# Kernel optimization log

Measured on AMD Instinct MI355X. Metric: run time of the kernel, lower is better.

Reference implementation:

```python
import math
import jax
import jax.numpy as jnp
import numpy as np

B = 4
SEQ_LEN = 512
ENC_IN = 21
TIME_DIM = 4
D_MODEL = 256
N_HEADS = 8
HEAD_DIM = D_MODEL // N_HEADS  # 32
NUM_K = 4
PATCH_LEN = 16
STRIDE = 8
EFF_LEN = (SEQ_LEN - PATCH_LEN) // STRIDE + 1  # 63, pad_len == 0
D_FF = 1024
PRED_LEN = 96
N_NEW = 2
N_ENC = 2
EPS = 1e-5


def setup_inputs() -> dict:
    key = jax.random.key(0)
    ks = iter(jax.random.split(key, 100))
    def nrm(shape, s=1.0):
        return jax.random.normal(next(ks), shape, jnp.float32) * s
    H, Dh, T, K = N_HEADS, HEAD_DIM, TIME_DIM, NUM_K
    inp = {}
    inp['x_enc'] = nrm((B, SEQ_LEN, ENC_IN))
    inp['x_mark_enc'] = jax.random.uniform(next(ks), (B, SEQ_LEN, TIME_DIM), jnp.float32)
    inp['x_dec'] = nrm((B, 144, ENC_IN))
    inp['x_mark_dec'] = jax.random.uniform(next(ks), (B, 144, TIME_DIM), jnp.float32)
    # DataEmbedding2: token conv (circular, k=3, no bias); positional enc is computed analytically
    inp['tok_W'] = nrm((D_MODEL, ENC_IN, 3), 0.05)
    # PatchEmbedding conv
    inp['patch_W'] = nrm((D_MODEL, D_MODEL, PATCH_LEN), 0.02)
    inp['patch_b'] = jnp.zeros((D_MODEL,), jnp.float32)
    # TimeKernelAttentionA layers (stacked on leading axis)
    inp['nl_WQ'] = nrm((N_NEW, D_MODEL, D_MODEL), 0.05)
    inp['nl_WK'] = nrm((N_NEW, D_MODEL, D_MODEL), 0.05)
    inp['nl_WV'] = nrm((N_NEW, D_MODEL, D_MODEL), 0.05)
    inp['nl_WO'] = nrm((N_NEW, D_MODEL, D_MODEL), 0.05)
    inp['nl_bO'] = jnp.zeros((N_NEW, D_MODEL), jnp.float32)
    inp['nl_mu_abs'] = nrm((N_NEW, H, Dh, T, K))
    inp['nl_sigma_abs'] = jnp.abs(nrm((N_NEW, H, Dh, T, K))) + 0.5
    inp['nl_w_abs'] = nrm((N_NEW, H, Dh, T, K), 0.1)
    inp['nl_mu_rel'] = nrm((N_NEW, H, Dh, T, K))
    inp['nl_sigma_rel'] = jnp.abs(nrm((N_NEW, H, Dh, T, K))) + 0.5
    inp['nl_w_rel'] = nrm((N_NEW, H, Dh, T, K), 0.1)
    inp['nl_alpha'] = jnp.ones((N_NEW, H), jnp.float32)
    inp['nl_beta'] = jnp.ones((N_NEW, H), jnp.float32)
    inp['nl_gamma'] = jnp.zeros((N_NEW, H), jnp.float32)
    # DataEmbedding_inverted: Linear(EFF_LEN -> d_model)
    inp['inv_W'] = nrm((D_MODEL, EFF_LEN), 0.05)
    inp['inv_b'] = jnp.zeros((D_MODEL,), jnp.float32)
    # Encoder layers (stacked)
    inp['el_Wq'] = nrm((N_ENC, D_MODEL, D_MODEL), 0.05)
    inp['el_bq'] = jnp.zeros((N_ENC, D_MODEL), jnp.float32)
    inp['el_Wk'] = nrm((N_ENC, D_MODEL, D_MODEL), 0.05)
    inp['el_bk'] = jnp.zeros((N_ENC, D_MODEL), jnp.float32)
    inp['el_Wv'] = nrm((N_ENC, D_MODEL, D_MODEL), 0.05)
    inp['el_bv'] = jnp.zeros((N_ENC, D_MODEL), jnp.float32)
    inp['el_Wo'] = nrm((N_ENC, D_MODEL, D_MODEL), 0.05)
    inp['el_bo'] = jnp.zeros((N_ENC, D_MODEL), jnp.float32)
    inp['el_W1'] = nrm((N_ENC, D_FF, D_MODEL), 0.05)
    inp['el_b1'] = jnp.zeros((N_ENC, D_FF), jnp.float32)
    inp['el_W2'] = nrm((N_ENC, D_MODEL, D_FF), 0.05)
    inp['el_b2'] = jnp.zeros((N_ENC, D_MODEL), jnp.float32)
    inp['el_n1_g'] = jnp.ones((N_ENC, D_MODEL), jnp.float32)
    inp['el_n1_b'] = jnp.zeros((N_ENC, D_MODEL), jnp.float32)
    inp['el_n2_g'] = jnp.ones((N_ENC, D_MODEL), jnp.float32)
    inp['el_n2_b'] = jnp.zeros((N_ENC, D_MODEL), jnp.float32)
    inp['norm_g'] = jnp.ones((D_MODEL,), jnp.float32)
    inp['norm_b'] = jnp.zeros((D_MODEL,), jnp.float32)
    inp['proj_W'] = nrm((PRED_LEN, D_MODEL), 0.05)
    inp['proj_b'] = jnp.zeros((PRED_LEN,), jnp.float32)
    return inp


def _conv1d(x, w, stride):
    # x: [B, Cin, L], w: [Cout, Cin, k]
    return jax.lax.conv_general_dilated(x, w, (stride,), 'VALID', dimension_numbers=('NCH', 'OIH', 'NCH'))


def _ln(x, g, b):
    m = x.mean(-1, keepdims=True)
    v = jnp.var(x, axis=-1, keepdims=True)
    return (x - m) / jnp.sqrt(v + EPS) * g + b


def _gauss(t, mu, sigma, w):
    # t: [B, N, T]; mu/sigma/w: [H, D, T, K] -> [B, H, D, N] (sum over T, K)
    diff = t[:, None, None, :, :, None] - mu[None, :, :, None, :, :]
    g = w[None, :, :, None, :, :] * jnp.exp(-(diff * diff) / (2.0 * sigma[None, :, :, None, :, :] ** 2))
    return g.sum((-1, -2))


def _tka(x, t, WQ, WK, WV, WO, bO, mu_a, sg_a, w_a, mu_r, sg_r, w_r, alpha, beta, gamma):
    Bn, L, _ = x.shape
    H, Dh = N_HEADS, HEAD_DIM
    q = (x @ WQ.T).reshape(Bn, L, H, Dh).transpose(0, 2, 1, 3)
    k = (x @ WK.T).reshape(Bn, L, H, Dh).transpose(0, 2, 1, 3)
    v = (x @ WV.T).reshape(Bn, L, H, Dh).transpose(0, 2, 1, 3)
    Xh = x.reshape(Bn, L, H, Dh).transpose(0, 2, 1, 3)
    Pij = jnp.einsum('bhid,bhjd->bhij', Xh, Xh)
    g_abs = _gauss(t, mu_a, sg_a, w_a)  # [B,H,D,L]
    t_rel = jnp.abs(t[:, :, None, :] - t[:, None, :, :]).reshape(Bn, L * L, TIME_DIM)
    g_rel = _gauss(t_rel, mu_r, sg_r, w_r).reshape(Bn, H, Dh, L, L).mean(2)  # [B,H,L,L]
    gi = g_abs.mean(2)  # [B,H,L]
    # NOTE: in the original, g_abs_j = g_abs_i.unsqueeze(-1).expand(...,L) (constant over j),
    # so (g_abs_i.unsqueeze(-1) + g_abs_j) == 2 * g_abs_i broadcast over j. We preserve that.
    a = alpha[None, :, None, None]
    b = beta[None, :, None, None]
    c = gamma[None, :, None, None]
    A = a * Pij * (2.0 * gi[..., None]) + b * Pij * g_rel + c
    scores = jnp.einsum('bhid,bhjd->bhij', q, k) / math.sqrt(Dh) * A
    attn = jax.nn.softmax(scores, axis=-1)
    out = jnp.einsum('bhij,bhjd->bhid', attn, v).transpose(0, 2, 1, 3).reshape(Bn, L, D_MODEL)
    return out @ WO.T + bO


def reference(x_enc, x_mark_enc, x_dec, x_mark_dec, tok_W, patch_W, patch_b, nl_WQ, nl_WK, nl_WV, nl_WO, nl_bO, nl_mu_abs, nl_sigma_abs, nl_w_abs, nl_mu_rel, nl_sigma_rel, nl_w_rel, nl_alpha, nl_beta, nl_gamma, inv_W, inv_b, el_Wq, el_bq, el_Wk, el_bk, el_Wv, el_bv, el_Wo, el_bo, el_W1, el_b1, el_W2, el_b2, el_n1_g, el_n1_b, el_n2_g, el_n2_b, norm_g, norm_b, proj_W, proj_b):
    # --- instance normalization (use_norm) ---
    means = x_enc.mean(1, keepdims=True)
    x = x_enc - means
    stdev = jnp.sqrt(jnp.var(x, axis=1, keepdims=True) + EPS)
    x = x / stdev
    # --- DataEmbedding2: TokenEmbedding (circular conv k=3) + sinusoidal PE, x_mark=None ---
    xc = x.transpose(0, 2, 1)  # [B, C, L]
    xp = jnp.concatenate([xc[:, :, -1:], xc, xc[:, :, :1]], axis=2)  # circular pad 1
    val = _conv1d(xp, tok_W, 1).transpose(0, 2, 1)  # [B, L, d]
    pos = jnp.arange(SEQ_LEN, dtype=jnp.float32)[:, None]
    div = jnp.exp(jnp.arange(0, D_MODEL, 2, dtype=jnp.float32) * (-math.log(10000.0) / D_MODEL))
    pe = jnp.zeros((SEQ_LEN, D_MODEL), jnp.float32)
    pe = pe.at[:, 0::2].set(jnp.sin(pos * div)).at[:, 1::2].set(jnp.cos(pos * div))
    enc = val + pe[None]
    # --- PatchEmbedding (pad_len == 0 for these dims) ---
    enc = _conv1d(enc.transpose(0, 2, 1), patch_W, STRIDE).transpose(0, 2, 1) + patch_b  # [B, 63, d]
    idx = jnp.arange(EFF_LEN)[:, None] * STRIDE + jnp.arange(PATCH_LEN)[None, :]
    t = x_mark_enc[:, idx, :].mean(2)  # [B, 63, T] (unfold + mean)
    # --- TimeKernelAttentionA stack ---
    for i in range(N_NEW):
        enc = _tka(enc, t, nl_WQ[i], nl_WK[i], nl_WV[i], nl_WO[i], nl_bO[i], nl_mu_abs[i], nl_sigma_abs[i], nl_w_abs[i], nl_mu_rel[i], nl_sigma_rel[i], nl_w_rel[i], nl_alpha[i], nl_beta[i], nl_gamma[i])
    # --- DataEmbedding_inverted ---
    xi = jnp.concatenate([enc.transpose(0, 2, 1), t.transpose(0, 2, 1)], axis=1)  # [B, d+T, 63]
    enc = xi @ inv_W.T + inv_b  # [B, d+T, d]
    # --- Encoder (FullAttention + FFN) ---
    Bn, Nt, _ = enc.shape
    for i in range(N_ENC):
        q = (enc @ el_Wq[i].T + el_bq[i]).reshape(Bn, Nt, N_HEADS, HEAD_DIM)
        k = (enc @ el_Wk[i].T + el_bk[i]).reshape(Bn, Nt, N_HEADS, HEAD_DIM)
        v = (enc @ el_Wv[i].T + el_bv[i]).reshape(Bn, Nt, N_HEADS, HEAD_DIM)
        sc = jnp.einsum('blhe,bshe->bhls', q, k) / math.sqrt(HEAD_DIM)
        attn = jax.nn.softmax(sc, axis=-1)
        o = jnp.einsum('bhls,bshd->blhd', attn, v).reshape(Bn, Nt, D_MODEL)
        o = o @ el_Wo[i].T + el_bo[i]
        xn = _ln(enc + o, el_n1_g[i], el_n1_b[i])
        y = jax.nn.gelu(xn @ el_W1[i].T + el_b1[i], approximate=False)
        y = y @ el_W2[i].T + el_b2[i]
        enc = _ln(xn + y, el_n2_g[i], el_n2_b[i])
    enc = _ln(enc, norm_g, norm_b)
    # --- projector + de-normalization ---
    dec = (enc @ proj_W.T + proj_b).transpose(0, 2, 1)[:, :, :ENC_IN]  # [B, pred_len, N]
    dec = dec * stdev[:, 0, :][:, None, :] + means[:, 0, :][:, None, :]
    return dec[:, -PRED_LEN:, :]
```

## Files before the change

kernel.cpp:

```cpp
#include <hip/hip_runtime.h>
#include <hip/hip_bf16.h>

#define NB 4
#define SEQ 512
#define CIN 21
#define TDIM 4
#define DM 256
#define NH 8
#define PLEN 16
#define PSTR 8
#define EL 63
#define DFF 1024
#define PRED 96
#define NT 260
#define EPSV 1e-5f

#define T_nlWQ 0
#define T_nlWK 131072
#define T_nlWV 262144
#define T_nlWO 393216
#define T_elWq 524288
#define T_elWk 655360
#define T_elWv 786432
#define T_elWo 917504
#define T_elW1 1048576
#define T_elW2 1572864
#define T_inv  2097152
#define T_proj 2113280
#define T_tok  2137856
#define T_pat  2153984

__device__ __forceinline__ float2 meanvar256(float v, float* sb) {
  __syncthreads();
  float s1 = v, s2 = v * v;
  #pragma unroll
  for (int off = 32; off > 0; off >>= 1) {
    s1 += __shfl_down(s1, off, 64);
    s2 += __shfl_down(s2, off, 64);
  }
  int wid = threadIdx.x >> 6, lane = threadIdx.x & 63;
  if (lane == 0) { sb[wid * 2] = s1; sb[wid * 2 + 1] = s2; }
  __syncthreads();
  float m = (sb[0] + sb[2] + sb[4] + sb[6]) * (1.0f / 256.0f);
  float q = (sb[1] + sb[3] + sb[5] + sb[7]) * (1.0f / 256.0f);
  return make_float2(m, q - m * m);
}

__device__ __forceinline__ void load16f(const float* p, float* o) {
  const float4* q = reinterpret_cast<const float4*>(p);
  float4 a = q[0], b = q[1], c = q[2], d = q[3];
  o[0]=a.x; o[1]=a.y; o[2]=a.z; o[3]=a.w;
  o[4]=b.x; o[5]=b.y; o[6]=b.z; o[7]=b.w;
  o[8]=c.x; o[9]=c.y; o[10]=c.z; o[11]=c.w;
  o[12]=d.x; o[13]=d.y; o[14]=d.z; o[15]=d.w;
}

__device__ __forceinline__ float dot32(const float4* a, const float4* b) {
  float s = 0.f;
  #pragma unroll
  for (int i = 0; i < 8; ++i) {
    float4 x = a[i], y = b[i];
    s += x.x*y.x + x.y*y.y + x.z*y.z + x.w*y.w;
  }
  return s;
}

__global__ void __launch_bounds__(256) k_prep(
    const float* __restrict__ nlWQ, const float* __restrict__ nlWK,
    const float* __restrict__ nlWV, const float* __restrict__ nlWO,
    const float* __restrict__ eWq, const float* __restrict__ eWk,
    const float* __restrict__ eWv, const float* __restrict__ eWo,
    const float* __restrict__ eW1, const float* __restrict__ eW2,
    const float* __restrict__ invW, const float* __restrict__ projW,
    const float* __restrict__ tokW, const float* __restrict__ patW,
    float* __restrict__ wt,
    const float* __restrict__ x, const float* __restrict__ xm,
    float* __restrict__ means, float* __restrict__ stdev,
    float* __restrict__ tout,
    const float* __restrict__ mu_r, const float* __restrict__ sg_r,
    const float* __restrict__ w_r,
    const float* __restrict__ mu_a, const float* __restrict__ sg_a,
    const float* __restrict__ w_a,
    float* __restrict__ grel, float* __restrict__ gib) {
  __shared__ float smem[32 * 33];
  int blk = blockIdx.x;
  int t = threadIdx.x;

  if (blk < 3128) {
    const float* src; float* dst; int R, C, tr, tc;
    if (blk < 1024) {
      int m = blk >> 6, tile = blk & 63;
      tr = tile >> 3; tc = tile & 7; R = 256; C = 256;
      int p = m >> 1, l = m & 1;
      const float* bases[8] = {nlWQ, nlWK, nlWV, nlWO, eWq, eWk, eWv, eWo};
      const int offs[8] = {T_nlWQ, T_nlWK, T_nlWV, T_nlWO, T_elWq, T_elWk, T_elWv, T_elWo};
      src = bases[p] + l * 65536;
      dst = wt + offs[p] + l * 65536;
    } else if (blk < 1536) {
      int q = blk - 1024; int l = q >> 8, s = q & 255;
      tr = s >> 3; tc = s & 7; R = 1024; C = 256;
      src = eW1 + l * 262144; dst = wt + T_elW1 + l * 262144;
    } else if (blk < 2048) {
      int q = blk - 1536; int l = q >> 8, s = q & 255;
      tr = s >> 5; tc = s & 31; R = 256; C = 1024;
      src = eW2 + l * 262144; dst = wt + T_elW2 + l * 262144;
    } else if (blk < 3072) {
      int q = blk - 2048; tr = q >> 7; tc = q & 127; R = 256; C = 4096;
      src = patW; dst = wt + T_pat;
    } else if (blk < 3088) {
      int q = blk - 3072; tr = q >> 1; tc = q & 1; R = 256; C = 63;
      src = invW; dst = wt + T_inv;
    } else if (blk < 3112) {
      int q = blk - 3088; tr = q >> 3; tc = q & 7; R = 96; C = 256;
      src = projW; dst = wt + T_proj;
    } else {
      int q = blk - 3112; tr = q >> 1; tc = q & 1; R = 256; C = 63;
      src = tokW; dst = wt + T_tok;
    }
    float (*ts)[33] = (float(*)[33])smem;
    int tx = t & 31, ty = t >> 5;
    #pragma unroll
    for (int i = 0; i < 4; ++i) {
      int r = tr * 32 + ty + i * 8, c = tc * 32 + tx;
      ts[ty + i * 8][tx] = (c < C) ? src[(size_t)r * C + c] : 0.f;
    }
    __syncthreads();
    #pragma unroll
    for (int i = 0; i < 4; ++i) {
      int c = tc * 32 + ty + i * 8, r = tr * 32 + tx;
      if (c < C) dst[(size_t)c * R + r] = ts[tx][ty + i * 8];
    }
  } else if (blk < 3216) {
    int sblk = blk - 3128;
    if (sblk < NB * CIN) {
      int b = sblk / CIN, c = sblk % CIN;
      const float* p = x + (size_t)b * SEQ * CIN + c;
      float v0 = p[t * CIN];
      float v1 = p[(t + 256) * CIN];
      float s1 = v0 + v1, s2 = v0 * v0 + v1 * v1;
      float* sb = smem;
      #pragma unroll
      for (int off = 32; off > 0; off >>= 1) {
        s1 += __shfl_down(s1, off, 64);
        s2 += __shfl_down(s2, off, 64);
      }
      int wid = t >> 6, lane = t & 63;
      if (lane == 0) { sb[wid * 2] = s1; sb[wid * 2 + 1] = s2; }
      __syncthreads();
      if (t == 0) {
        float a = sb[0] + sb[2] + sb[4] + sb[6];
        float q = sb[1] + sb[3] + sb[5] + sb[7];
        float m = a * (1.0f / 512.0f);
        float var = q * (1.0f / 512.0f) - m * m;
        means[sblk] = m;
        stdev[sblk] = sqrtf(var + EPSV);
      }
    } else {
      int idx = (sblk - NB * CIN) * 256 + t;
      if (idx >= NB * EL * TDIM) return;
      int b = idx / (EL * TDIM), r = idx % (EL * TDIM);
      int l = r >> 2, ti = r & 3;
      const float* p = xm + (size_t)b * SEQ * TDIM + (size_t)l * PSTR * TDIM + ti;
      float s = 0.f;
      #pragma unroll
      for (int k = 0; k < PLEN; ++k) s += p[k * TDIM];
      tout[idx] = s * (1.f / 16.f);
    }
  } else {
    int gblk = blk - 3216;
    int L = gblk / (NB * 252);
    int rem0 = gblk % (NB * 252);
    int b = rem0 / 252, chunk = rem0 % 252;
    int po = L * 4096;
    float* grelL = grel + (size_t)L * (NB * NH * EL * EL);
    float* gibL  = gib + (size_t)L * (NB * NH * EL);
    int h = t >> 5, dh = t & 31;
    float* s_t = smem;
    if (t < EL * TDIM) {
      int l = t >> 2, ti = t & 3;
      const float* p = xm + (size_t)b * SEQ * TDIM + (size_t)l * PSTR * TDIM + ti;
      float s = 0.f;
      #pragma unroll
      for (int k = 0; k < PLEN; ++k) s += p[k * TDIM];
      s_t[t] = s * (1.f / 16.f);
    }
    float pm[16], pc[16], pw[16];
    load16f(mu_r + po + (size_t)t * 16, pm);
    load16f(sg_r + po + (size_t)t * 16, pc);
    load16f(w_r  + po + (size_t)t * 16, pw);
    #pragma unroll
    for (int p = 0; p < 16; ++p) pc[p] = -0.5f / (pc[p] * pc[p]);
    __syncthreads();
    #pragma unroll 1
    for (int q = 0; q < 8; ++q) {
      int p = chunk * 8 + q;
      int i = (int)((127.0f - sqrtf(16129.0f - 8.0f * (float)p)) * 0.5f);
      while (i * (127 - i) / 2 > p) --i;
      while ((i + 1) * (126 - i) / 2 <= p) ++i;
      int j = i + (p - i * (127 - i) / 2);
      float dvv[4];
      dvv[0] = fabsf(s_t[i*4+0] - s_t[j*4+0]);
      dvv[1] = fabsf(s_t[i*4+1] - s_t[j*4+1]);
      dvv[2] = fabsf(s_t[i*4+2] - s_t[j*4+2]);
      dvv[3] = fabsf(s_t[i*4+3] - s_t[j*4+3]);
      float srel = 0.f;
      #pragma unroll
      for (int tt = 0; tt < 4; ++tt)
        #pragma unroll
        for (int k = 0; k < 4; ++k) {
          int pp = tt * 4 + k;
          float df = dvv[tt] - pm[pp];
          srel += pw[pp] * __expf(pc[pp] * df * df);
        }
      #pragma unroll
      for (int m = 1; m < 32; m <<= 1) srel += __shfl_xor(srel, m, 64);
      if (dh == 0) {
        float v = srel * (1.f / 32.f);
        grelL[(((size_t)b * NH + h) * EL + i) * EL + j] = v;
        grelL[(((size_t)b * NH + h) * EL + j) * EL + i] = v;
      }
    }
    if (chunk < EL) {
      load16f(mu_a + po + (size_t)t * 16, pm);
      load16f(sg_a + po + (size_t)t * 16, pc);
      load16f(w_a  + po + (size_t)t * 16, pw);
      #pragma unroll
      for (int p = 0; p < 16; ++p) pc[p] = -0.5f / (pc[p] * pc[p]);
      int i = chunk;
      float tiv[4] = {s_t[i*4+0], s_t[i*4+1], s_t[i*4+2], s_t[i*4+3]};
      float sabs = 0.f;
      #pragma unroll
      for (int tt = 0; tt < 4; ++tt)
        #pragma unroll
        for (int k = 0; k < 4; ++k) {
          int pp = tt * 4 + k;
          float df = tiv[tt] - pm[pp];
          sabs += pw[pp] * __expf(pc[pp] * df * df);
        }
      #pragma unroll
      for (int m = 1; m < 32; m <<= 1) sabs += __shfl_xor(sabs, m, 64);
      if (dh == 0) gibL[((size_t)b * NH + h) * EL + i] = sabs * (1.f / 32.f);
    }
  }
}

__global__ void __launch_bounds__(256) k_tokconv(
    const float* __restrict__ x, const float* __restrict__ tokWT,
    const float* __restrict__ means, const float* __restrict__ stdev,
    float* __restrict__ enc1) {
  int bi = blockIdx.x;
  int b = bi >> 6, sg = bi & 63;
  int s0 = sg * 8;
  __shared__ float sxr[10 * CIN];
  int t = threadIdx.x;
  if (t < 10 * CIN) {
    int li = t / CIN, c = t % CIN;
    int row = (s0 - 1 + li + SEQ) & 511;
    sxr[t] = (x[(size_t)b * SEQ * CIN + row * CIN + c] - means[b * CIN + c])
             / stdev[b * CIN + c];
  }
  __syncthreads();
  int d = t;
  float wreg[63];
  #pragma unroll
  for (int q = 0; q < 63; ++q) wreg[q] = tokWT[q * DM + d];
  int de = d & ~1;
  float dv = expf((float)de * (-9.210340371976184f / 256.0f));
  bool isodd = (d & 1);
  #pragma unroll 1
  for (int k = 0; k < 8; ++k) {
    float acc = 0.f;
    const float* sr = sxr + k * CIN;
    #pragma unroll
    for (int c = 0; c < CIN; ++c) {
      acc += sr[c]           * wreg[c * 3 + 0];
      acc += sr[CIN + c]     * wreg[c * 3 + 1];
      acc += sr[2 * CIN + c] * wreg[c * 3 + 2];
    }
    float ang = (float)(s0 + k) * dv;
    float pe = isodd ? cosf(ang) : sinf(ang);
    enc1[((size_t)b * SEQ + s0 + k) * DM + d] = acc + pe;
  }
}

__global__ void __launch_bounds__(256) k_patch_part(
    const float* __restrict__ enc1, const float* __restrict__ pWT,
    float* __restrict__ pbuf) {
  int bi = blockIdx.x;
  int pg = bi >> 3, kc = bi & 7;
  int p0 = pg * 6;
  __shared__ __align__(16) float sA[6 * 32 * 20];
  int t = threadIdx.x;
  for (int idx = t; idx < 6 * 32 * PLEN; idx += 256) {
    int pp = idx >> 9;
    int rem = idx & 511;
    int c = rem >> 4, k = rem & 15;
    int p = p0 + pp;
    int b = p / EL, l = p % EL;
    sA[pp * 640 + c * 20 + k] =
        enc1[((size_t)b * SEQ + l * PSTR + k) * DM + kc * 32 + c];
  }
  __syncthreads();
  int d = t;
  const float* wb = pWT + (size_t)(kc * 32 * PLEN) * DM + d;
  float acc[6] = {0.f, 0.f, 0.f, 0.f, 0.f, 0.f};
  #pragma unroll 1
  for (int kk0 = 0; kk0 < 512; kk0 += 8) {
    float w[8];
    #pragma unroll
    for (int q = 0; q < 8; ++q) w[q] = wb[(size_t)(kk0 + q) * DM];
    #pragma unroll
    for (int q = 0; q < 8; ++q) {
      int kk = kk0 + q;
      const float* sa = sA + (kk >> 4) * 20 + (kk & 15);
      acc[0] += sa[0 * 640] * w[q];
      acc[1] += sa[1 * 640] * w[q];
      acc[2] += sa[2 * 640] * w[q];
      acc[3] += sa[3 * 640] * w[q];
      acc[4] += sa[4 * 640] * w[q];
      acc[5] += sa[5 * 640] * w[q];
    }
  }
  const int S = NB * EL * DM;
  #pragma unroll
  for (int pp = 0; pp < 6; ++pp)
    pbuf[(size_t)kc * S + (size_t)(p0 + pp) * DM + d] = acc[pp];
}

__global__ void k_patch_red(const float* __restrict__ pbuf, const float* __restrict__ pb,
                            float* __restrict__ encP) {
  int p = blockIdx.x, t = threadIdx.x;
  const int S = NB * EL * DM;
  float v = 0.f;
  #pragma unroll
  for (int s = 0; s < 8; ++s) v += pbuf[(size_t)s * S + (size_t)p * DM + t];
  encP[(size_t)p * DM + t] = v + pb[t];
}

template<int R>
__global__ void __launch_bounds__(256) k_qkv2(
    const float* __restrict__ WqT, const float* __restrict__ WkT,
    const float* __restrict__ WvT,
    const float* __restrict__ bq, const float* __restrict__ bk,
    const float* __restrict__ bv,
    const float* __restrict__ xin,
    float* __restrict__ qo, float* __restrict__ ko, float* __restrict__ vo) {
  int bi = blockIdx.x;
  int rg = bi / 3, mat = bi % 3;
  int row0 = rg * R;
  __shared__ __align__(16) float sx[R * DM];
  __shared__ __align__(16) float sp[3 * R * DM];
  int t = threadIdx.x;
  int colg = t & 63, kq = t >> 6;
  #pragma unroll
  for (int i = 0; i < R / 4; ++i)
    reinterpret_cast<float4*>(sx)[t + i * 256] =
        reinterpret_cast<const float4*>(xin + (size_t)row0 * DM)[t + i * 256];
  __syncthreads();
  const float* WT = (mat == 0) ? WqT : (mat == 1) ? WkT : WvT;
  const float* bias = (mat == 0) ? bq : (mat == 1) ? bk : bv;
  float* out = (mat == 0) ? qo : (mat == 1) ? ko : vo;
  float acc[R][4];
  #pragma unroll
  for (int r = 0; r < R; ++r) { acc[r][0]=0.f; acc[r][1]=0.f; acc[r][2]=0.f; acc[r][3]=0.f; }
  const float* xb = sx + kq * 64;
  const float4* wp = reinterpret_cast<const float4*>(WT + (size_t)(kq * 64) * DM) + colg;
  #pragma unroll 1
  for (int k0 = 0; k0 < 64; k0 += 4) {
    float4 w[4];
    #pragma unroll
    for (int q = 0; q < 4; ++q) w[q] = wp[(size_t)(k0 + q) * 64];
    #pragma unroll
    for (int q = 0; q < 4; ++q)
      #pragma unroll
      for (int r = 0; r < R; ++r) {
        float xv = xb[r * DM + k0 + q];
        acc[r][0] += xv * w[q].x; acc[r][1] += xv * w[q].y;
        acc[r][2] += xv * w[q].z; acc[r][3] += xv * w[q].w;
      }
  }
  if (kq) {
    #pragma unroll
    for (int r = 0; r < R; ++r)
      reinterpret_cast<float4*>(sp)[((kq - 1) * R + r) * 64 + colg] =
          make_float4(acc[r][0], acc[r][1], acc[r][2], acc[r][3]);
  }
  __syncthreads();
  if (kq == 0) {
    float4 b4 = bias ? reinterpret_cast<const float4*>(bias)[colg]
                     : make_float4(0.f, 0.f, 0.f, 0.f);
    const float4* sp4 = reinterpret_cast<const float4*>(sp);
    #pragma unroll
    for (int r = 0; r < R; ++r) {
      float4 p0 = sp4[(0 * R + r) * 64 + colg];
      float4 p1 = sp4[(1 * R + r) * 64 + colg];
      float4 p2 = sp4[(2 * R + r) * 64 + colg];
      float4 o;
      o.x = acc[r][0] + p0.x + p1.x + p2.x + b4.x;
      o.y = acc[r][1] + p0.y + p1.y + p2.y + b4.y;
      o.z = acc[r][2] + p0.z + p1.z + p2.z + b4.z;
      o.w = acc[r][3] + p0.w + p1.w + p2.w + b4.w;
      reinterpret_cast<float4*>(out + (size_t)(row0 + r) * DM)[colg] = o;
    }
  }
}

__global__ void __launch_bounds__(256) k_qkv_l1(
    const float* __restrict__ WqT, const float* __restrict__ WkT,
    const float* __restrict__ WvT,
    const float* __restrict__ bq, const float* __restrict__ bk,
    const float* __restrict__ bv,
    const float* __restrict__ xin,
    float* __restrict__ qo, float* __restrict__ ko, float* __restrict__ vo) {
  int bi = blockIdx.x;
  const float* WT; const float* bias; float* out; int row0;
  if (bi < 130)      { WT = WkT; bias = bk; out = ko; row0 = bi * 8; }
  else if (bi < 260) { WT = WvT; bias = bv; out = vo; row0 = (bi - 130) * 8; }
  else {
    int gq = bi - 260;
    WT = WqT; bias = bq; out = qo;
    row0 = (gq / 3) * NT + (gq % 3) * 8;
  }
  __shared__ __align__(16) float sx[8 * DM];
  __shared__ __align__(16) float sp[3 * 8 * DM];
  int t = threadIdx.x;
  int colg = t & 63, kq = t >> 6;
  #pragma unroll
  for (int i = 0; i < 2; ++i)
    reinterpret_cast<float4*>(sx)[t + i * 256] =
        reinterpret_cast<const float4*>(xin + (size_t)row0 * DM)[t + i * 256];
  __syncthreads();
  float acc[8][4];
  #pragma unroll
  for (int r = 0; r < 8; ++r) { acc[r][0]=0.f; acc[r][1]=0.f; acc[r][2]=0.f; acc[r][3]=0.f; }
  const float* xb = sx + kq * 64;
  const float4* wp = reinterpret_cast<const float4*>(WT + (size_t)(kq * 64) * DM) + colg;
  #pragma unroll 1
  for (int k0 = 0; k0 < 64; k0 += 4) {
    float4 w[4];
    #pragma unroll
    for (int q = 0; q < 4; ++q) w[q] = wp[(size_t)(k0 + q) * 64];
    #pragma unroll
    for (int q = 0; q < 4; ++q)
      #pragma unroll
      for (int r = 0; r < 8; ++r) {
        float xv = xb[r * DM + k0 + q];
        acc[r][0] += xv * w[q].x; acc[r][1] += xv * w[q].y;
        acc[r][2] += xv * w[q].z; acc[r][3] += xv * w[q].w;
      }
  }
  if (kq) {
    #pragma unroll
    for (int r = 0; r < 8; ++r)
      reinterpret_cast<float4*>(sp)[((kq - 1) * 8 + r) * 64 + colg] =
          make_float4(acc[r][0], acc[r][1], acc[r][2], acc[r][3]);
  }
  __syncthreads();
  if (kq == 0) {
    float4 b4 = reinterpret_cast<const float4*>(bias)[colg];
    const float4* sp4 = reinterpret_cast<const float4*>(sp);
    #pragma unroll
    for (int r = 0; r < 8; ++r) {
      float4 p0 = sp4[(0 * 8 + r) * 64 + colg];
      float4 p1 = sp4[(1 * 8 + r) * 64 + colg];
      float4 p2 = sp4[(2 * 8 + r) * 64 + colg];
      float4 o;
      o.x = acc[r][0] + p0.x + p1.x + p2.x + b4.x;
      o.y = acc[r][1] + p0.y + p1.y + p2.y + b4.y;
      o.z = acc[r][2] + p0.z + p1.z + p2.z + b4.z;
      o.w = acc[r][3] + p0.w + p1.w + p2.w + b4.w;
      reinterpret_cast<float4*>(out + (size_t)(row0 + r) * DM)[colg] = o;
    }
  }
}

__global__ void __launch_bounds__(512) k_tka_attn_f(
    const float* __restrict__ xin, const float* __restrict__ qw,
    const float* __restrict__ kw, const float* __restrict__ vw,
    const float* __restrict__ grel, const float* __restrict__ gib,
    const float* __restrict__ alpha, const float* __restrict__ beta,
    const float* __restrict__ gamma,
    const float* __restrict__ WOT, const float* __restrict__ bO,
    float* __restrict__ xout) {
  int bi = blockIdx.x;
  int b = bi / EL, i = bi % EL;
  int t = threadIdx.x;
  __shared__ __align__(16) float sQX[2 * DM];
  __shared__ float sP[NH * 64];
  __shared__ __align__(16) float sO[DM];
  __shared__ float sPV[DM];
  if (t < 2 * DM)
    sQX[t] = (t < DM) ? qw[(size_t)bi * DM + t] : xin[(size_t)bi * DM + (t - DM)];
  __syncthreads();
  {
    int tile = t >> 8, h = (t >> 5) & 7, jj = t & 31;
    int j = tile * 32 + jj;
    bool valid = (j < EL);
    int jc = valid ? j : (EL - 1);
    float gi = gib[((size_t)b * NH + h) * EL + i];
    float al = alpha[h], be = beta[h], ga = gamma[h];
    const float* grow = grel + (((size_t)b * NH + h) * EL + i) * EL;
    const float4* kp = reinterpret_cast<const float4*>(
        kw + (size_t)(b * EL + jc) * DM + h * 32);
    const float4* xp = reinterpret_cast<const float4*>(
        xin + (size_t)(b * EL + jc) * DM + h * 32);
    float4 kf[8], xf[8];
    #pragma unroll
    for (int q = 0; q < 8; ++q) { kf[q] = kp[q]; xf[q] = xp[q]; }
    float qk  = dot32(reinterpret_cast<const float4*>(sQX + h * 32), kf);
    float pij = dot32(reinterpret_cast<const float4*>(sQX + DM + h * 32), xf);
    float A = al * pij * (2.f * gi) + be * pij * grow[jc] + ga;
    const float scale = 0.17677669529663687f;
    sP[h * 64 + tile * 32 + jj] = valid ? (qk * scale * A) : -1e30f;
  }
  __syncthreads();
  {
    int h = t >> 6, dh = t & 63;
    float v = sP[h * 64 + dh];
    float m = v;
    #pragma unroll
    for (int s = 1; s < 64; s <<= 1) m = fmaxf(m, __shfl_xor(m, s, 64));
    float e = __expf(v - m);
    float ssum = e;
    #pragma unroll
    for (int s = 1; s < 64; s <<= 1) ssum += __shfl_xor(ssum, s, 64);
    sP[h * 64 + dh] = e / ssum;
  }
  __syncthreads();
  {
    int ch = t & 255, jh = t >> 8, hh = ch >> 5;
    float acc = 0.f;
    const float* pp = sP + hh * 64 + jh * 32;
    int jbase = jh * 32;
    #pragma unroll 1
    for (int j0 = 0; j0 < 32; j0 += 8) {
      float v[8];
      #pragma unroll
      for (int q = 0; q < 8; ++q) {
        int jx = jbase + j0 + q;
        if (jx > 62) jx = 62;
        v[q] = vw[(size_t)(b * EL + jx) * DM + ch];
      }
      #pragma unroll
      for (int q = 0; q < 8; ++q) acc += pp[j0 + q] * v[q];
    }
    if (jh) sPV[ch] = acc;
    __syncthreads();
    if (!jh) sO[ch] = acc + sPV[ch];
  }
  __syncthreads();
  {
    int col = t & 255, kh = t >> 8;
    float acc = 0.f;
    const float* wc = WOT + (size_t)(kh * 128) * DM + col;
    const float* sx = sO + kh * 128;
    #pragma unroll 1
    for (int k0 = 0; k0 < 128; k0 += 8) {
      float w[8];
      #pragma unroll
      for (int q = 0; q < 8; ++q) w[q] = wc[(size_t)(k0 + q) * DM];
      #pragma unroll
      for (int q = 0; q < 8; ++q) acc += sx[k0 + q] * w[q];
    }
    if (kh) sPV[col] = acc;
    __syncthreads();
    if (!kh) xout[(size_t)bi * DM + col] = acc + sPV[col] + bO[col];
  }
}

__global__ void k_invemb(const float* __restrict__ invWT, const float* __restrict__ invb,
                         const float* __restrict__ encP, const float* __restrict__ tws,
                         float* __restrict__ enc2) {
  int bi = blockIdx.x;
  int b = bi / NT, n = bi % NT;
  __shared__ float sx[EL];
  int t = threadIdx.x;
  if (t < EL) {
    sx[t] = (n < DM) ? encP[(size_t)(b * EL + t) * DM + n]
                     : tws[b * EL * TDIM + t * TDIM + (n - DM)];
  }
  __syncthreads();
  float acc = 0.f;
  #pragma unroll 1
  for (int l0 = 0; l0 < 63; l0 += 9) {
    float w[9];
    #pragma unroll
    for (int q = 0; q < 9; ++q) w[q] = invWT[(size_t)(l0 + q) * DM + t];
    #pragma unroll
    for (int q = 0; q < 9; ++q) acc += sx[l0 + q] * w[q];
  }
  enc2[(size_t)bi * DM + t] = acc + invb[t];
}

__global__ void __launch_bounds__(512) k_enc_attn_f(
    const float* __restrict__ qw, const float* __restrict__ kw,
    const float* __restrict__ vw,
    const float* __restrict__ WoT, const float* __restrict__ bo,
    const float* __restrict__ g, const float* __restrict__ bb,
    const float* __restrict__ resin, float* __restrict__ out, int tpb) {
  int blk = blockIdx.x;
  int b = blk / tpb, it = blk % tpb;
  int i0 = it * 4;
  int t = threadIdx.x;

  __shared__ __align__(16) float sQ[4 * DM];
  __shared__ float sS[4 * NH * NT];
  __shared__ float sL[4 * NH];
  __shared__ __align__(16) float sPV[4 * DM];
  __shared__ float sb[8];

  for (int idx = t; idx < 4 * DM; idx += 512)
    sQ[idx] = qw[((size_t)(b * NT + i0)) * DM + idx];
  __syncthreads();

  const float scale = 0.17677669529663687f;
  {
    int half = t >> 8, h = (t >> 5) & 7, jj = t & 31;
    for (int tile = half; tile < 9; tile += 2) {
      int j = tile * 32 + jj;
      if (j >= NT) break;
      const float4* kp = reinterpret_cast<const float4*>(
          kw + ((size_t)(b * NT + j)) * DM + h * 32);
      float4 kf[8];
      #pragma unroll
      for (int q = 0; q < 8; ++q) kf[q] = kp[q];
      #pragma unroll
      for (int i = 0; i < 4; ++i) {
        float s = dot32(reinterpret_cast<const float4*>(sQ + i * DM + h * 32), kf);
        sS[(i * NH + h) * NT + j] = s * scale;
      }
    }
  }
  __syncthreads();
  {
    int combo = t >> 4, lane16 = t & 15;
    float* row = sS + (size_t)combo * NT;
    float m = -1e30f;
    for (int jx = lane16; jx < NT; jx += 16) m = fmaxf(m, row[jx]);
    #pragma unroll
    for (int s = 1; s < 16; s <<= 1) m = fmaxf(m, __shfl_xor(m, s, 16));
    float ssum = 0.f;
    for (int jx = lane16; jx < NT; jx += 16) {
      float e = __expf(row[jx] - m);
      row[jx] = e;
      ssum += e;
    }
    #pragma unroll
    for (int s = 1; s < 16; s <<= 1) ssum += __shfl_xor(ssum, s, 16);
    if (lane16 == 0) sL[combo] = ssum;
  }
  __syncthreads();
  {
    int ch = t & 255, jh = t >> 8, hh = ch >> 5;
    float o0 = 0.f, o1 = 0.f, o2 = 0.f, o3 = 0.f;
    const float* vbase = vw + ((size_t)(b * NT + jh * 130)) * DM + ch;
    const float* p0 = sS + (0 * NH + hh) * NT + jh * 130;
    const float* p1 = sS + (1 * NH + hh) * NT + jh * 130;
    const float* p2 = sS + (2 * NH + hh) * NT + jh * 130;
    const float* p3 = sS + (3 * NH + hh) * NT + jh * 130;
    #pragma unroll 1
    for (int j0 = 0; j0 < 130; j0 += 10) {
      float v[10];
      #pragma unroll
      for (int q = 0; q < 10; ++q) v[q] = vbase[(size_t)(j0 + q) * DM];
      #pragma unroll
      for (int q = 0; q < 10; ++q) {
        o0 += p0[j0 + q] * v[q]; o1 += p1[j0 + q] * v[q];
        o2 += p2[j0 + q] * v[q]; o3 += p3[j0 + q] * v[q];
      }
    }
    if (jh) {
      sPV[0 * DM + ch] = o0; sPV[1 * DM + ch] = o1;
      sPV[2 * DM + ch] = o2; sPV[3 * DM + ch] = o3;
    }
    __syncthreads();
    if (!jh) {
      sQ[0 * DM + ch] = (o0 + sPV[0 * DM + ch]) / sL[0 * NH + hh];
      sQ[1 * DM + ch] = (o1 + sPV[1 * DM + ch]) / sL[1 * NH + hh];
      sQ[2 * DM + ch] = (o2 + sPV[2 * DM + ch]) / sL[2 * NH + hh];
      sQ[3 * DM + ch] = (o3 + sPV[3 * DM + ch]) / sL[3 * NH + hh];
    }
  }
  __syncthreads();
  {
    int col = t & 255, kh = t >> 8;
    float acc[4] = {0.f, 0.f, 0.f, 0.f};
    const float* wcol = WoT + (size_t)(kh * 128) * DM + col;
    const float* s0 = sQ + kh * 128;
    #pragma unroll 1
    for (int k0 = 0; k0 < 128; k0 += 8) {
      float w[8];
      #pragma unroll
      for (int q = 0; q < 8; ++q) w[q] = wcol[(size_t)(k0 + q) * DM];
      #pragma unroll
      for (int q = 0; q < 8; ++q) {
        acc[0] += s0[0 * DM + k0 + q] * w[q];
        acc[1] += s0[1 * DM + k0 + q] * w[q];
        acc[2] += s0[2 * DM + k0 + q] * w[q];
        acc[3] += s0[3 * DM + k0 + q] * w[q];
      }
    }
    if (kh) {
      sPV[0 * DM + col] = acc[0]; sPV[1 * DM + col] = acc[1];
      sPV[2 * DM + col] = acc[2]; sPV[3 * DM + col] = acc[3];
    }
    __syncthreads();
    float ov[4] = {0.f, 0.f, 0.f, 0.f};
    float gg = g[col], bb2 = bb[col];
    if (!kh) {
      float bias = bo[col];
      #pragma unroll
      for (int r = 0; r < 4; ++r)
        ov[r] = acc[r] + sPV[r * DM + col] + bias
              + resin[((size_t)(b * NT + i0 + r)) * DM + col];
    }
    int wid = t >> 6, lane = t & 63;
    #pragma unroll 1
    for (int r = 0; r < 4; ++r) {
      float o = (!kh) ? ov[r] : 0.f;
      __syncthreads();
      float s1 = o, s2 = o * o;
      #pragma unroll
      for (int off = 32; off > 0; off >>= 1) {
        s1 += __shfl_down(s1, off, 64);
        s2 += __shfl_down(s2, off, 64);
      }
      if (lane == 0 && wid < 4) { sb[wid * 2] = s1; sb[wid * 2 + 1] = s2; }
      __syncthreads();
      float m = (sb[0] + sb[2] + sb[4] + sb[6]) * (1.f / 256.f);
      float q2 = (sb[1] + sb[3] + sb[5] + sb[7]) * (1.f / 256.f);
      float var = q2 - m * m;
      if (!kh)
        out[((size_t)(b * NT + i0 + r)) * DM + col] =
            (ov[r] - m) * rsqrtf(var + EPSV) * gg + bb2;
    }
  }
}

__global__ void __launch_bounds__(256) k_ffnf(
    const float* __restrict__ W1T, const float* __restrict__ b1,
    const float* __restrict__ W2T, const float* __restrict__ b2,
    const float* __restrict__ g, const float* __restrict__ bb,
    const float* __restrict__ xn, float* __restrict__ out, int gpb) {
  int blk = blockIdx.x;
  int row0 = gpb ? ((blk / gpb) * NT + (blk % gpb) * 4) : blk * 4;
  __shared__ __align__(16) float sx[4 * DM];
  __shared__ __align__(16) float sy[4 * DFF];
  __shared__ __align__(16) float sp[3 * 4 * DM];
  int t = threadIdx.x;
  int colg = t & 63, kq = t >> 6;
  reinterpret_cast<float4*>(sx)[t] =
      reinterpret_cast<const float4*>(xn + (size_t)row0 * DM)[t];
  __syncthreads();

  #pragma unroll 1
  for (int fg = 0; fg < 4; ++fg) {
    float acc[4][4];
    #pragma unroll
    for (int r = 0; r < 4; ++r) { acc[r][0]=0.f; acc[r][1]=0.f; acc[r][2]=0.f; acc[r][3]=0.f; }
    const float* xb = sx + kq * 64;
    const float4* wp = reinterpret_cast<const float4*>(W1T + (size_t)(kq * 64) * DFF)
                       + (fg * 64 + colg);
    #pragma unroll 1
    for (int k0 = 0; k0 < 64; k0 += 4) {
      float4 w[4];
      #pragma unroll
      for (int q = 0; q < 4; ++q) w[q] = wp[(size_t)(k0 + q) * 256];
      #pragma unroll
      for (int q = 0; q < 4; ++q)
        #pragma unroll
        for (int r = 0; r < 4; ++r) {
          float xv = xb[r * DM + k0 + q];
          acc[r][0] += xv * w[q].x; acc[r][1] += xv * w[q].y;
          acc[r][2] += xv * w[q].z; acc[r][3] += xv * w[q].w;
        }
    }
    if (kq) {
      #pragma unroll
      for (int r = 0; r < 4; ++r)
        reinterpret_cast<float4*>(sp)[((kq - 1) * 4 + r) * 64 + colg] =
            make_float4(acc[r][0], acc[r][1], acc[r][2], acc[r][3]);
    }
    __syncthreads();
    if (kq == 0) {
      float4 b4 = *reinterpret_cast<const float4*>(b1 + fg * 256 + colg * 4);
      const float4* sp4 = reinterpret_cast<const float4*>(sp);
      #pragma unroll
      for (int r = 0; r < 4; ++r) {
        float4 p0 = sp4[(0 * 4 + r) * 64 + colg];
        float4 p1 = sp4[(1 * 4 + r) * 64 + colg];
        float4 p2 = sp4[(2 * 4 + r) * 64 + colg];
        float a0 = acc[r][0] + p0.x + p1.x + p2.x + b4.x;
        float a1 = acc[r][1] + p0.y + p1.y + p2.y + b4.y;
        float a2 = acc[r][2] + p0.z + p1.z + p2.z + b4.z;
        float a3 = acc[r][3] + p0.w + p1.w + p2.w + b4.w;
        float4 o;
        o.x = 0.5f * a0 * (1.f + erff(a0 * 0.70710678118654752f));
        o.y = 0.5f * a1 * (1.f + erff(a1 * 0.70710678118654752f));
        o.z = 0.5f * a2 * (1.f + erff(a2 * 0.70710678118654752f));
        o.w = 0.5f * a3 * (1.f + erff(a3 * 0.70710678118654752f));
        reinterpret_cast<float4*>(sy)[r * 256 + fg * 64 + colg] = o;
      }
    }
    __syncthreads();
  }

  float acc[4][4];
  #pragma unroll
  for (int r = 0; r < 4; ++r) { acc[r][0]=0.f; acc[r][1]=0.f; acc[r][2]=0.f; acc[r][3]=0.f; }
  const float* yb = sy + kq * 256;
  const float4* wp = reinterpret_cast<const float4*>(W2T + (size_t)(kq * 256) * DM) + colg;
  #pragma unroll 1
  for (int k0 = 0; k0 < 256; k0 += 8) {
    float4 w[8];
    #pragma unroll
    for (int q = 0; q < 8; ++q) w[q] = wp[(size_t)(k0 + q) * 64];
    #pragma unroll
    for (int q = 0; q < 8; ++q)
      #pragma unroll
      for (int r = 0; r < 4; ++r) {
        float yv = yb[r * DFF + k0 + q];
        acc[r][0] += yv * w[q].x; acc[r][1] += yv * w[q].y;
        acc[r][2] += yv * w[q].z; acc[r][3] += yv * w[q].w;
      }
  }
  if (kq) {
    #pragma unroll
    for (int r = 0; r < 4; ++r)
      reinterpret_cast<float4*>(sp)[((kq - 1) * 4 + r) * 64 + colg] =
          make_float4(acc[r][0], acc[r][1], acc[r][2], acc[r][3]);
  }
  __syncthreads();
  if (kq == 0) {
    float4 b4 = reinterpret_cast<const float4*>(b2)[colg];
    float4 g4 = reinterpret_cast<const float4*>(g)[colg];
    float4 bb4 = reinterpret_cast<const float4*>(bb)[colg];
    const float4* sp4 = reinterpret_cast<const float4*>(sp);
    #pragma unroll 1
    for (int r = 0; r < 4; ++r) {
      float4 p0 = sp4[(0 * 4 + r) * 64 + colg];
      float4 p1 = sp4[(1 * 4 + r) * 64 + colg];
      float4 p2 = sp4[(2 * 4 + r) * 64 + colg];
      float4 xr = reinterpret_cast<const float4*>(sx)[r * 64 + colg];
      float o0 = acc[r][0] + p0.x + p1.x + p2.x + b4.x + xr.x;
      float o1 = acc[r][1] + p0.y + p1.y + p2.y + b4.y + xr.y;
      float o2 = acc[r][2] + p0.z + p1.z + p2.z + b4.z + xr.z;
      float o3 = acc[r][3] + p0.w + p1.w + p2.w + b4.w + xr.w;
      float s1 = o0 + o1 + o2 + o3;
      float s2 = o0*o0 + o1*o1 + o2*o2 + o3*o3;
      #pragma unroll
      for (int m = 1; m < 64; m <<= 1) {
        s1 += __shfl_xor(s1, m, 64);
        s2 += __shfl_xor(s2, m, 64);
      }
      float mean = s1 * (1.f / 256.f);
      float var = s2 * (1.f / 256.f) - mean * mean;
      float rs = rsqrtf(var + EPSV);
      float4 o;
      o.x = (o0 - mean) * rs * g4.x + bb4.x;
      o.y = (o1 - mean) * rs * g4.y + bb4.y;
      o.z = (o2 - mean) * rs * g4.z + bb4.z;
      o.w = (o3 - mean) * rs * g4.w + bb4.w;
      reinterpret_cast<float4*>(out + (size_t)(row0 + r) * DM)[colg] = o;
    }
  }
}

__global__ void k_final(const float* __restrict__ g, const float* __restrict__ bb,
                        const float* __restrict__ pWT, const float* __restrict__ pb,
                        const float* __restrict__ enc2,
                        const float* __restrict__ stdev, const float* __restrict__ means,
                        float* __restrict__ out) {
  int bi = blockIdx.x;
  int b = bi / CIN, c = bi % CIN;
  __shared__ __align__(16) float sx[DM];
  __shared__ float sb[8];
  int t = threadIdx.x;
  float v = enc2[(size_t)(b * NT + c) * DM + t];
  float2 mv = meanvar256(v, sb);
  sx[t] = (v - mv.x) * rsqrtf(mv.y + EPSV) * g[t] + bb[t];
  __syncthreads();
  if (t < PRED) {
    float acc = 0.f;
    #pragma unroll 1
    for (int k0 = 0; k0 < DM; k0 += 8) {
      float w[8];
      #pragma unroll
      for (int q = 0; q < 8; ++q) w[q] = pWT[(size_t)(k0 + q) * PRED + t];
      #pragma unroll
      for (int q = 0; q < 8; ++q) acc += sx[k0 + q] * w[q];
    }
    float y = (acc + pb[t]) * stdev[bi] + means[bi];
    out[(size_t)b * PRED * CIN + t * CIN + c] = y;
  }
}

extern "C" void kernel_launch(void* const* d_in, const int* in_sizes, int n_in,
                              void* d_out, int out_size, void* d_ws, size_t ws_size,
                              hipStream_t stream) {
  const float* x_enc   = (const float*)d_in[0];
  const float* x_mark  = (const float*)d_in[1];
  const float* tok_W   = (const float*)d_in[4];
  const float* patch_W = (const float*)d_in[5];
  const float* patch_b = (const float*)d_in[6];
  const float* nl_WQ   = (const float*)d_in[7];
  const float* nl_WK   = (const float*)d_in[8];
  const float* nl_WV   = (const float*)d_in[9];
  const float* nl_WO   = (const float*)d_in[10];
  const float* nl_bO   = (const float*)d_in[11];
  const float* nl_mu_a = (const float*)d_in[12];
  const float* nl_sg_a = (const float*)d_in[13];
  const float* nl_w_a  = (const float*)d_in[14];
  const float* nl_mu_r = (const float*)d_in[15];
  const float* nl_sg_r = (const float*)d_in[16];
  const float* nl_w_r  = (const float*)d_in[17];
  const float* nl_al   = (const float*)d_in[18];
  const float* nl_be   = (const float*)d_in[19];
  const float* nl_ga   = (const float*)d_in[20];
  const float* inv_W   = (const float*)d_in[21];
  const float* inv_b   = (const float*)d_in[22];
  const float* el_Wq   = (const float*)d_in[23];
  const float* el_bq   = (const float*)d_in[24];
  const float* el_Wk   = (const float*)d_in[25];
  const float* el_bk   = (const float*)d_in[26];
  const float* el_Wv   = (const float*)d_in[27];
  const float* el_bv   = (const float*)d_in[28];
  const float* el_Wo   = (const float*)d_in[29];
  const float* el_bo   = (const float*)d_in[30];
  const float* el_W1   = (const float*)d_in[31];
  const float* el_b1   = (const float*)d_in[32];
  const float* el_W2   = (const float*)d_in[33];
  const float* el_b2   = (const float*)d_in[34];
  const float* n1g     = (const float*)d_in[35];
  const float* n1b     = (const float*)d_in[36];
  const float* n2g     = (const float*)d_in[37];
  const float* n2b     = (const float*)d_in[38];
  const float* norm_g  = (const float*)d_in[39];
  const float* norm_b  = (const float*)d_in[40];
  const float* proj_W  = (const float*)d_in[41];
  const float* proj_b  = (const float*)d_in[42];

  float* ws = (float*)d_ws;
  float* means = ws + 0;
  float* stdev = ws + 96;
  float* tws   = ws + 192;
  float* enc1  = ws + 1216;
  float* encP  = ws + 525504;
  float* pbuf  = ws + 590016;
  float* enc2  = ws + 1106112;
  float* qb    = ws + 1638592;
  float* kb    = ws + 1904832;
  float* vb    = ws + 2171072;
  float* encPb = ws + 3502272;
  float* grel  = ws + 4567232;
  float* gib   = ws + 4821248;
  float* wsT   = ws + 4825344;
  float* xn    = qb;

  k_prep<<<5232, 256, 0, stream>>>(nl_WQ, nl_WK, nl_WV, nl_WO,
                                   el_Wq, el_Wk, el_Wv, el_Wo,
                                   el_W1, el_W2, inv_W, proj_W,
                                   tok_W, patch_W, wsT,
                                   x_enc, x_mark, means, stdev, tws,
                                   nl_mu_r, nl_sg_r, nl_w_r,
                                   nl_mu_a, nl_sg_a, nl_w_a, grel, gib);
  k_tokconv<<<NB * 64, 256, 0, stream>>>(x_enc, wsT + T_tok, means, stdev, enc1);
  k_patch_part<<<42 * 8, 256, 0, stream>>>(enc1, wsT + T_pat, pbuf);
  k_patch_red<<<NB * EL, 256, 0, stream>>>(pbuf, patch_b, encP);

  for (int L = 0; L < 2; ++L) {
    size_t wo = (size_t)L * DM * DM;
    const float* xi = L ? encPb : encP;
    float* xo       = L ? encP : encPb;
    k_qkv2<4><<<63 * 3, 256, 0, stream>>>(wsT + T_nlWQ + wo, wsT + T_nlWK + wo,
                                          wsT + T_nlWV + wo,
                                          nullptr, nullptr, nullptr,
                                          xi, qb, kb, vb);
    k_tka_attn_f<<<NB * EL, 512, 0, stream>>>(xi, qb, kb, vb,
        grel + (size_t)L * (NB * NH * EL * EL), gib + (size_t)L * (NB * NH * EL),
        nl_al + L * 8, nl_be + L * 8, nl_ga + L * 8,
        wsT + T_nlWO + wo, nl_bO + L * DM, xo);
  }

  k_invemb<<<NB * NT, 256, 0, stream>>>(wsT + T_inv, inv_b, encP, tws, enc2);

  k_qkv2<8><<<130 * 3, 256, 0, stream>>>(wsT + T_elWq, wsT + T_elWk, wsT + T_elWv,
                                         el_bq, el_bk, el_bv,
                                         enc2, qb, kb, vb);
  k_enc_attn_f<<<NB * 65, 512, 0, stream>>>(qb, kb, vb, wsT + T_elWo, el_bo,
                                            n1g, n1b, enc2, xn, 65);
  k_ffnf<<<260, 256, 0, stream>>>(wsT + T_elW1, el_b1, wsT + T_elW2, el_b2,
                                  n2g, n2b, xn, enc2, 0);

  {
    size_t wo = (size_t)DM * DM;
    size_t bo = (size_t)DM;
    size_t fo = (size_t)DFF * DM;
    k_qkv_l1<<<272, 256, 0, stream>>>(wsT + T_elWq + wo, wsT + T_elWk + wo,
                                      wsT + T_elWv + wo,
                                      el_bq + bo, el_bk + bo, el_bv + bo,
                                      enc2, qb, kb, vb);
    k_enc_attn_f<<<NB * 6, 512, 0, stream>>>(qb, kb, vb, wsT + T_elWo + wo,
                                             el_bo + bo, n1g + bo, n1b + bo,
                                             enc2, xn, 6);
    k_ffnf<<<NB * 6, 256, 0, stream>>>(wsT + T_elW1 + fo, el_b1 + DFF,
                                       wsT + T_elW2 + fo, el_b2 + bo,
                                       n2g + bo, n2b + bo, xn, enc2, 6);
  }

  k_final<<<NB * CIN, 256, 0, stream>>>(norm_g, norm_b, wsT + T_proj, proj_b,
                                        enc2, stdev, means, (float*)d_out);
}
```

Before: 467.6 us.

## Split fused FFN into two kernels for more parallelism per stage

```diff
diff --git a/kernel.cpp b/kernel.cpp
--- a/kernel.cpp
+++ b/kernel.cpp
@@ -737,81 +737,93 @@
   }
 }
 
-__global__ void __launch_bounds__(256) k_ffnf(
+__global__ void __launch_bounds__(256) k_ffn1(
     const float* __restrict__ W1T, const float* __restrict__ b1,
+    const float* __restrict__ xn, float* __restrict__ y1, int gpb) {
+  int bi = blockIdx.x;
+  int rg = bi >> 2, fg = bi & 3;
+  int row0 = gpb ? ((rg / gpb) * NT + (rg % gpb) * 8) : rg * 8;
+  __shared__ __align__(16) float sx[8 * DM];
+  __shared__ __align__(16) float sp[3 * 8 * DM];
+  int t = threadIdx.x;
+  int colg = t & 63, kq = t >> 6;
+  #pragma unroll
+  for (int i = 0; i < 2; ++i)
+    reinterpret_cast<float4*>(sx)[t + i * 256] =
+        reinterpret_cast<const float4*>(xn + (size_t)row0 * DM)[t + i * 256];
+  __syncthreads();
+  int f = fg * 256 + colg * 4;
+  float acc[8][4];
+  #pragma unroll
+  for (int r = 0; r < 8; ++r) { acc[r][0]=0.f; acc[r][1]=0.f; acc[r][2]=0.f; acc[r][3]=0.f; }
+  const float* xb = sx + kq * 64;
+  const float4* wp = reinterpret_cast<const float4*>(W1T + (size_t)(kq * 64) * DFF + f);
+  #pragma unroll 1
+  for (int k0 = 0; k0 < 64; k0 += 4) {
+    float4 w[4];
+    #pragma unroll
+    for (int q = 0; q < 4; ++q) w[q] = wp[(size_t)(k0 + q) * 256];
+    #pragma unroll
+    for (int q = 0; q < 4; ++q)
+      #pragma unroll
+      for (int r = 0; r < 8; ++r) {
+        float xv = xb[r * DM + k0 + q];
+        acc[r][0] += xv * w[q].x; acc[r][1] += xv * w[q].y;
+        acc[r][2] += xv * w[q].z; acc[r][3] += xv * w[q].w;
+      }
+  }
+  if (kq) {
+    #pragma unroll
+    for (int r = 0; r < 8; ++r)
+      reinterpret_cast<float4*>(sp)[((kq - 1) * 8 + r) * 64 + colg] =
+          make_float4(acc[r][0], acc[r][1], acc[r][2], acc[r][3]);
+  }
+  __syncthreads();
+  if (kq == 0) {
+    float4 b4 = *reinterpret_cast<const float4*>(b1 + f);
+    const float4* sp4 = reinterpret_cast<const float4*>(sp);
+    #pragma unroll 1
+    for (int r = 0; r < 8; ++r) {
+      float4 p0 = sp4[(0 * 8 + r) * 64 + colg];
+      float4 p1 = sp4[(1 * 8 + r) * 64 + colg];
+      float4 p2 = sp4[(2 * 8 + r) * 64 + colg];
+      float a0 = acc[r][0] + p0.x + p1.x + p2.x + b4.x;
+      float a1 = acc[r][1] + p0.y + p1.y + p2.y + b4.y;
+      float a2 = acc[r][2] + p0.z + p1.z + p2.z + b4.z;
+      float a3 = acc[r][3] + p0.w + p1.w + p2.w + b4.w;
+      float4 o;
+      o.x = 0.5f * a0 * (1.f + erff(a0 * 0.70710678118654752f));
+      o.y = 0.5f * a1 * (1.f + erff(a1 * 0.70710678118654752f));
+      o.z = 0.5f * a2 * (1.f + erff(a2 * 0.70710678118654752f));
+      o.w = 0.5f * a3 * (1.f + erff(a3 * 0.70710678118654752f));
+      *reinterpret_cast<float4*>(y1 + (size_t)(row0 + r) * DFF + f) = o;
+    }
+  }
+}
+
+__global__ void __launch_bounds__(512) k_ffn2f(
     const float* __restrict__ W2T, const float* __restrict__ b2,
     const float* __restrict__ g, const float* __restrict__ bb,
-    const float* __restrict__ xn, float* __restrict__ out, int gpb) {
+    const float* __restrict__ y1, const float* __restrict__ xn,
+    float* __restrict__ out, int gpb) {
   int blk = blockIdx.x;
   int row0 = gpb ? ((blk / gpb) * NT + (blk % gpb) * 4) : blk * 4;
-  __shared__ __align__(16) float sx[4 * DM];
   __shared__ __align__(16) float sy[4 * DFF];
-  __shared__ __align__(16) float sp[3 * 4 * DM];
+  __shared__ __align__(16) float sp[7 * 4 * DM];
   int t = threadIdx.x;
   int colg = t & 63, kq = t >> 6;
-  reinterpret_cast<float4*>(sx)[t] =
-      reinterpret_cast<const float4*>(xn + (size_t)row0 * DM)[t];
-  __syncthreads();
-
+  #pragma unroll
+  for (int i = 0; i < 2; ++i)
+    reinterpret_cast<float4*>(sy)[t + i * 512] =
+        reinterpret_cast<const float4*>(y1 + (size_t)row0 * DFF)[t + i * 512];
+  __syncthreads();
+  float acc[4][4];
+  #pragma unroll
+  for (int r = 0; r < 4; ++r) { acc[r][0]=0.f; acc[r][1]=0.f; acc[r][2]=0.f; acc[r][3]=0.f; }
+  const float* yb = sy + kq * 128;
+  const float4* wp = reinterpret_cast<const float4*>(W2T + (size_t)(kq * 128) * DM) + colg;
   #pragma unroll 1
-  for (int fg = 0; fg < 4; ++fg) {
-    float acc[4][4];
-    #pragma unroll
-    for (int r = 0; r < 4; ++r) { acc[r][0]=0.f; acc[r][1]=0.f; acc[r][2]=0.f; acc[r][3]=0.f; }
-    const float* xb = sx + kq * 64;
-    const float4* wp = reinterpret_cast<const float4*>(W1T + (size_t)(kq * 64) * DFF)
-                       + (fg * 64 + colg);
-    #pragma unroll 1
-    for (int k0 = 0; k0 < 64; k0 += 4) {
-      float4 w[4];
-      #pragma unroll
-      for (int q = 0; q < 4; ++q) w[q] = wp[(size_t)(k0 + q) * 256];
-      #pragma unroll
-      for (int q = 0; q < 4; ++q)
-        #pragma unroll
-        for (int r = 0; r < 4; ++r) {
-          float xv = xb[r * DM + k0 + q];
-          acc[r][0] += xv * w[q].x; acc[r][1] += xv * w[q].y;
-          acc[r][2] += xv * w[q].z; acc[r][3] += xv * w[q].w;
-        }
-    }
-    if (kq) {
-      #pragma unroll
-      for (int r = 0; r < 4; ++r)
-        reinterpret_cast<float4*>(sp)[((kq - 1) * 4 + r) * 64 + colg] =
-            make_float4(acc[r][0], acc[r][1], acc[r][2], acc[r][3]);
-    }
-    __syncthreads();
-    if (kq == 0) {
-      float4 b4 = *reinterpret_cast<const float4*>(b1 + fg * 256 + colg * 4);
-      const float4* sp4 = reinterpret_cast<const float4*>(sp);
-      #pragma unroll
-      for (int r = 0; r < 4; ++r) {
-        float4 p0 = sp4[(0 * 4 + r) * 64 + colg];
-        float4 p1 = sp4[(1 * 4 + r) * 64 + colg];
-        float4 p2 = sp4[(2 * 4 + r) * 64 + colg];
-        float a0 = acc[r][0] + p0.x + p1.x + p2.x + b4.x;
-        float a1 = acc[r][1] + p0.y + p1.y + p2.y + b4.y;
-        float a2 = acc[r][2] + p0.z + p1.z + p2.z + b4.z;
-        float a3 = acc[r][3] + p0.w + p1.w + p2.w + b4.w;
-        float4 o;
-        o.x = 0.5f * a0 * (1.f + erff(a0 * 0.70710678118654752f));
-        o.y = 0.5f * a1 * (1.f + erff(a1 * 0.70710678118654752f));
-        o.z = 0.5f * a2 * (1.f + erff(a2 * 0.70710678118654752f));
-        o.w = 0.5f * a3 * (1.f + erff(a3 * 0.70710678118654752f));
-        reinterpret_cast<float4*>(sy)[r * 256 + fg * 64 + colg] = o;
-      }
-    }
-    __syncthreads();
-  }
-
-  float acc[4][4];
-  #pragma unroll
-  for (int r = 0; r < 4; ++r) { acc[r][0]=0.f; acc[r][1]=0.f; acc[r][2]=0.f; acc[r][3]=0.f; }
-  const float* yb = sy + kq * 256;
-  const float4* wp = reinterpret_cast<const float4*>(W2T + (size_t)(kq * 256) * DM) + colg;
-  #pragma unroll 1
-  for (int k0 = 0; k0 < 256; k0 += 8) {
+  for (int k0 = 0; k0 < 128; k0 += 8) {
     float4 w[8];
     #pragma unroll
     for (int q = 0; q < 8; ++q) w[q] = wp[(size_t)(k0 + q) * 64];
@@ -838,14 +850,14 @@
     const float4* sp4 = reinterpret_cast<const float4*>(sp);
     #pragma unroll 1
     for (int r = 0; r < 4; ++r) {
-      float4 p0 = sp4[(0 * 4 + r) * 64 + colg];
-      float4 p1 = sp4[(1 * 4 + r) * 64 + colg];
-      float4 p2 = sp4[(2 * 4 + r) * 64 + colg];
-      float4 xr = reinterpret_cast<const float4*>(sx)[r * 64 + colg];
-      float o0 = acc[r][0] + p0.x + p1.x + p2.x + b4.x + xr.x;
-      float o1 = acc[r][1] + p0.y + p1.y + p2.y + b4.y + xr.y;
-      float o2 = acc[r][2] + p0.z + p1.z + p2.z + b4.z + xr.z;
-      float o3 = acc[r][3] + p0.w + p1.w + p2.w + b4.w + xr.w;
+      float o0 = acc[r][0], o1 = acc[r][1], o2 = acc[r][2], o3 = acc[r][3];
+      #pragma unroll
+      for (int s = 0; s < 7; ++s) {
+        float4 ps = sp4[(s * 4 + r) * 64 + colg];
+        o0 += ps.x; o1 += ps.y; o2 += ps.z; o3 += ps.w;
+      }
+      float4 xr = reinterpret_cast<const float4*>(xn + (size_t)(row0 + r) * DM)[colg];
+      o0 += b4.x + xr.x; o1 += b4.y + xr.y; o2 += b4.z + xr.z; o3 += b4.w + xr.w;
       float s1 = o0 + o1 + o2 + o3;
       float s2 = o0*o0 + o1*o1 + o2*o2 + o3*o3;
       #pragma unroll
@@ -951,6 +963,7 @@
   float* qb    = ws + 1638592;
   float* kb    = ws + 1904832;
   float* vb    = ws + 2171072;
+  float* y1    = ws + 2437312;
   float* encPb = ws + 3502272;
   float* grel  = ws + 4567232;
   float* gib   = ws + 4821248;
@@ -989,8 +1002,8 @@
                                          enc2, qb, kb, vb);
   k_enc_attn_f<<<NB * 65, 512, 0, stream>>>(qb, kb, vb, wsT + T_elWo, el_bo,
                                             n1g, n1b, enc2, xn, 65);
-  k_ffnf<<<260, 256, 0, stream>>>(wsT + T_elW1, el_b1, wsT + T_elW2, el_b2,
-                                  n2g, n2b, xn, enc2, 0);
+  k_ffn1<<<130 * 4, 256, 0, stream>>>(wsT + T_elW1, el_b1, xn, y1, 0);
+  k_ffn2f<<<260, 512, 0, stream>>>(wsT + T_elW2, el_b2, n2g, n2b, y1, xn, enc2, 0);
 
   {
     size_t wo = (size_t)DM * DM;
@@ -1003,9 +1016,9 @@
     k_enc_attn_f<<<NB * 6, 512, 0, stream>>>(qb, kb, vb, wsT + T_elWo + wo,
                                              el_bo + bo, n1g + bo, n1b + bo,
                                              enc2, xn, 6);
-    k_ffnf<<<NB * 6, 256, 0, stream>>>(wsT + T_elW1 + fo, el_b1 + DFF,
-                                       wsT + T_elW2 + fo, el_b2 + bo,
-                                       n2g + bo, n2b + bo, xn, enc2, 6);
+    k_ffn1<<<12 * 4, 256, 0, stream>>>(wsT + T_elW1 + fo, el_b1 + DFF, xn, y1, 3);
+    k_ffn2f<<<NB * 6, 512, 0, stream>>>(wsT + T_elW2 + fo, el_b2 + bo,
+                                        n2g + bo, n2b + bo, y1, xn, enc2, 6);
   }
 
   k_final<<<NB * CIN, 256, 0, stream>>>(norm_g, norm_b, wsT + T_proj, proj_b,
```

Measured after the change: 423.6 us. 9.4% less time.
